# Optimization experiments

Measured on AMD Instinct MI355X. Metric: run time of the kernel, lower is better.

The kernel has to match this reference:

```python
import jax, jax.numpy as jnp
import numpy as np

B = 524288      # batch
CONT = 64       # continuous features
N_CATE = 16     # categorical fields
VOCAB = 1000    # vocab per field
EM = 8          # embedding dim
LOW = EM * N_CATE + CONT  # 192
R = 32          # representation dim
RH = 32         # rep hidden dim
PH = 16         # head hidden dim
N_HEAD = 8      # number of routing heads


def setup_inputs() -> dict:
    key = jax.random.key(0)
    ks = jax.random.split(key, 16)
    s = 0.05
    return {
        "x_cont": jax.random.normal(ks[0], (B, CONT), dtype=jnp.float32),
        "x_cate": jax.random.randint(ks[1], (B, N_CATE), 0, VOCAB, dtype=jnp.int64),
        "t": jax.random.randint(ks[2], (B, 1), 0, N_HEAD, dtype=jnp.int64),
        # embedding tables, one per categorical field
        "emb": jax.random.normal(ks[3], (N_CATE, VOCAB, EM), dtype=jnp.float32) * s,
        # representation DNN: LOW -> RH -> RH -> R (2 hidden layers + output)
        "W1": jax.random.normal(ks[4], (LOW, RH), dtype=jnp.float32) * s,
        "b1": jnp.zeros((RH,), dtype=jnp.float32),
        "W2": jax.random.normal(ks[5], (RH, RH), dtype=jnp.float32) * s,
        "b2": jnp.zeros((RH,), dtype=jnp.float32),
        "W3": jax.random.normal(ks[6], (RH, R), dtype=jnp.float32) * s,
        "b3": jnp.zeros((R,), dtype=jnp.float32),
        # stacked per-head DNNs: R -> PH -> 1 (1 hidden layer + output)
        "HW1": jax.random.normal(ks[7], (N_HEAD, R, PH), dtype=jnp.float32) * s,
        "Hb1": jnp.zeros((N_HEAD, PH), dtype=jnp.float32),
        "HW2": jax.random.normal(ks[8], (N_HEAD, PH, 1), dtype=jnp.float32) * s,
        "Hb2": jnp.zeros((N_HEAD, 1), dtype=jnp.float32),
    }


def reference(x_cont, x_cate, t, emb, W1, b1, W2, b2, W3, b3, HW1, Hb1, HW2, Hb2):
    # LowFeature: embed each categorical field and concat with continuous
    # emb[f, x_cate[:, f]] -> [B, N_CATE, EM]
    e = emb[jnp.arange(N_CATE)[None, :], x_cate]
    x = jnp.concatenate([x_cont, e.reshape(e.shape[0], -1)], axis=1)  # [B, LOW]
    # representation DNN (eval mode: dropout is identity)
    h = jax.nn.relu(x @ W1 + b1)
    h = jax.nn.relu(h @ W2 + b2)
    r = h @ W3 + b3  # [B, R]
    # evaluate all heads batched, then gather the routed head per sample
    hh = jax.nn.relu(jnp.einsum('br,nrh->bnh', r, HW1) + Hb1[None])  # [B, N_HEAD, PH]
    y_all = jnp.einsum('bnh,nho->bno', hh, HW2) + Hb2[None]          # [B, N_HEAD, 1]
    y = jnp.take_along_axis(y_all[..., 0], t, axis=1)[:, 0]          # [B]
    return y
```

## Files before the change

kernel.cpp:

```cpp
#include <hip/hip_runtime.h>

namespace {

typedef float  f32x4  __attribute__((ext_vector_type(4)));
typedef float  f32x16 __attribute__((ext_vector_type(16)));
typedef short  bf16x8 __attribute__((ext_vector_type(8)));
typedef int    i32x4  __attribute__((ext_vector_type(4)));
typedef unsigned int u32;

constexpr int kRows  = 524288;
constexpr int kCont  = 64;
constexpr int kNCate = 16;
constexpr int kVocab = 1000;
constexpr int kEm    = 8;
constexpr int kRH    = 32;
constexpr int kPH    = 16;

constexpr int    kNFrag = 48;
constexpr size_t kOffEH = (size_t)kNFrag * 1024;

__device__ inline u32 rne_hi(float x) {
    u32 u = __float_as_uint(x);
    return ((u + 0x7fffu + ((u >> 16) & 1u)) >> 16) & 0xffffu;
}
__device__ inline float hi_f32(u32 h) { return __uint_as_float(h << 16); }
__device__ inline u32 pack2(float a, float b) {
    return rne_hi(a) | (rne_hi(b) << 16);
}

union FragU { u32 w[4]; bf16x8 v; uint4 u4; };

__device__ inline f32x16 mfma16(bf16x8 a, bf16x8 b, f32x16 c) {
    return __builtin_amdgcn_mfma_f32_32x32x16_bf16(a, b, c, 0, 0, 0);
}
__device__ inline f32x16 zero16() {
    f32x16 z;
#pragma unroll
    for (int i = 0; i < 16; ++i) z[i] = 0.f;
    return z;
}
__device__ inline void gload_lds16(const void* g, void* l) {
    __builtin_amdgcn_global_load_lds(
        (const __attribute__((address_space(1))) void*)g,
        (__attribute__((address_space(3))) void*)l, 16, 0, 0);
}

__global__ __launch_bounds__(256) void build_wfrags(
    const float* __restrict__ W1, const float* __restrict__ W2,
    const float* __restrict__ W3, const float* __restrict__ HW1,
    ushort* __restrict__ WF)
{
    int gid = blockIdx.x * blockDim.x + threadIdx.x;
    if (gid >= kNFrag * 64) return;
    const int q = gid >> 6, l = gid & 63;
    const int lc = l & 31, g = l >> 5;

    const float* src; int k0, col, ldn, p;
    if (q < 12) {
        src = W1; col = lc; ldn = 32; p = 0;
        k0 = (q < 4) ? (16*q + 8*g) : (64 + 8*(q - 4) + 64*g);
    } else if (q < 24) {
        int f = q - 12;
        src = W1; col = lc; ldn = 32; p = 1;
        k0 = (f < 4) ? (16*f + 8*g) : (64 + 8*(f - 4) + 64*g);
    }
    else if (q < 28) { int u2 = q-24; src = W2; k0 = 16*(u2>>1) + 8*g; col = lc; ldn = 32; p = u2&1; }
    else if (q < 32) { int u2 = q-28; src = W3; k0 = 16*(u2>>1) + 8*g; col = lc; ldn = 32; p = u2&1; }
    else {
        int u2 = q-32; int n = u2>>2; int f = (u2>>1)&1; p = u2&1;
        int c128 = n*32 + lc; int head = c128 >> 4, ph = c128 & 15;
        src = HW1 + (size_t)head * kRH * kPH + ph;
        k0 = 16*f + 8*g; col = 0; ldn = kPH;
    }

    u32 hv[8];
#pragma unroll
    for (int j = 0; j < 8; ++j) {
        float w = src[(size_t)(k0 + j) * ldn + col];
        u32 h = rne_hi(w);
        hv[j] = (p == 0) ? h : rne_hi(w - hi_f32(h));
    }
    FragU fu;
#pragma unroll
    for (int w = 0; w < 4; ++w) fu.w[w] = hv[2*w] | (hv[2*w+1] << 16);
    ((uint4*)WF)[q * 64 + l] = fu.u4;
}

__global__ __launch_bounds__(256) void build_embhi(
    const float* __restrict__ emb, ushort* __restrict__ eh)
{
    int r = blockIdx.x * blockDim.x + threadIdx.x;
    if (r >= kNCate * kVocab) return;
    const float* e = emb + (size_t)r * kEm;
    FragU H;
#pragma unroll
    for (int w = 0; w < 4; ++w)
        H.w[w] = pack2(e[2*w], e[2*w+1]);
    ((uint4*)eh)[r] = H.u4;
}

__device__ inline void transition(const float* v, int g, FragU* H, FragU* L) {
    u32 hw[8], lw[8];
#pragma unroll
    for (int p = 0; p < 8; ++p) {
        float v0 = v[2*p], v1 = v[2*p+1];
        u32 h0 = rne_hi(v0), h1 = rne_hi(v1);
        hw[p] = h0 | (h1 << 16);
        lw[p] = pack2(v0 - hi_f32(h0), v1 - hi_f32(h1));
    }
#pragma unroll
    for (int f2 = 0; f2 < 2; ++f2) {
        u32 hp[4], lp[4];
#pragma unroll
        for (int p = 0; p < 4; ++p) {
            hp[p] = (u32)__shfl_xor((int)hw[4*f2 + p], 32);
            lp[p] = (u32)__shfl_xor((int)lw[4*f2 + p], 32);
        }
        H[f2].w[0] = g ? hp[2] : hw[4*f2+0];
        H[f2].w[1] = g ? hp[3] : hw[4*f2+1];
        H[f2].w[2] = g ? hw[4*f2+2] : hp[0];
        H[f2].w[3] = g ? hw[4*f2+3] : hp[1];
        L[f2].w[0] = g ? lp[2] : lw[4*f2+0];
        L[f2].w[1] = g ? lp[3] : lw[4*f2+1];
        L[f2].w[2] = g ? lw[4*f2+2] : lp[0];
        L[f2].w[3] = g ? lw[4*f2+3] : lp[1];
    }
}

__global__ __launch_bounds__(256, 2) void fused_main(
    const float* __restrict__ xc, const int* __restrict__ xcate,
    const int* __restrict__ tptr,
    const ushort* __restrict__ WF,
    const ushort* __restrict__ eh,
    const float* __restrict__ b1, const float* __restrict__ b2,
    const float* __restrict__ b3, const float* __restrict__ Hb1,
    const float* __restrict__ HW2, const float* __restrict__ Hb2,
    float* __restrict__ out)
{
    __shared__ __align__(16) uint4 sW4[16 * 64];
    __shared__ __align__(16) float sX[4][2048];
    __shared__ __align__(16) float sB[360];

    const int tid = threadIdx.x;
    const uint4* wf4 = (const uint4*)WF;

#pragma unroll
    for (int it = 0; it < 4; ++it) {
        const int i = tid + 256 * it;
        sW4[i] = wf4[i];
    }
    for (int i = tid; i < 360; i += 256) {
        float v;
        if      (i < 32)  v = b1[i];
        else if (i < 64)  v = b2[i - 32];
        else if (i < 96)  v = b3[i - 64];
        else if (i < 224) v = Hb1[i - 96];
        else if (i < 352) v = HW2[i - 224];
        else              v = Hb2[i - 352];
        sB[i] = v;
    }
    __syncthreads();

    const int wv = tid >> 6, l = tid & 63;
    const int lc = l & 31, g = l >> 5;
    const int tb = blockIdx.x * 128 + wv * 32;
    const int arow = tb + lc;

    char* xb = (char*)&sX[wv][0];
    {
        const float* xbase = xc + (size_t)tb * kCont;
#pragma unroll
        for (int i = 0; i < 8; ++i) {
            const int r   = 4*i + (l >> 4);
            const int c4s = (l & 15) ^ (r & 15);
            gload_lds16(xbase + r * kCont + c4s * 4, xb + i * 1024);
        }
    }

    i32x4 iq[2];
    {
        const i32x4* cr4 = (const i32x4*)(xcate + (size_t)arow * kNCate + 8*g);
        iq[0] = cr4[0];
        iq[1] = cr4[1];
    }
    const int t_lane = tptr[arow];

    uint4 ehv[8];
    {
        const uint4* eh4 = (const uint4*)eh;
#pragma unroll
        for (int i = 0; i < 8; ++i) {
            const int c   = i + 8*g;
            const int idx = (i < 4) ? iq[0][i] : iq[1][i - 4];
            ehv[i] = eh4[(size_t)(c * kVocab + idx)];
        }
    }

    asm volatile("s_waitcnt vmcnt(0)" ::: "memory");
    __builtin_amdgcn_sched_barrier(0);

    f32x16 acca = zero16(), accb = zero16();
#pragma unroll
    for (int f = 0; f < 4; ++f) {
        const int c0 = 4*f + 2*g;
        f32x4 va0 = *(const f32x4*)(xb + lc*256 + (((c0)     ^ (lc & 15)) * 16));
        f32x4 va1 = *(const f32x4*)(xb + lc*256 + (((c0 + 1) ^ (lc & 15)) * 16));
        FragU H, L;
#pragma unroll
        for (int w = 0; w < 4; ++w) {
            const f32x4& va = (w < 2) ? va0 : va1;
            const float v0 = va[2*(w & 1)], v1 = va[2*(w & 1) + 1];
            u32 h0 = rne_hi(v0), h1 = rne_hi(v1);
            H.w[w] = h0 | (h1 << 16);
            L.w[w] = pack2(v0 - hi_f32(h0), v1 - hi_f32(h1));
        }
        FragU WH, WL;
        WH.u4 = sW4[f * 64 + l];
        WL.u4 = sW4[(12 + f) * 64 + l];
        f32x16& acc = (f & 1) ? accb : acca;
        acc = mfma16(WH.v, H.v, acc);
        acc = mfma16(WL.v, H.v, acc);
        acc = mfma16(WH.v, L.v, acc);
    }
#pragma unroll
    for (int i = 0; i < 8; ++i) {
        const int f = 4 + i;
        FragU BH, WH;
        BH.u4 = ehv[i];
        WH.u4 = sW4[f * 64 + l];
        f32x16& acc = (f & 1) ? accb : acca;
        acc = mfma16(WH.v, BH.v, acc);
    }

    float v1v[16];
    {
#pragma unroll
        for (int p = 0; p < 4; ++p) {
            f32x4 bq = *(const f32x4*)&sB[0 + 8*p + 4*g];
#pragma unroll
            for (int m = 0; m < 4; ++m)
                v1v[4*p + m] = fmaxf(acca[4*p + m] + accb[4*p + m] + bq[m], 0.f);
        }
    }
    FragU a2h[2], a2l[2];
    transition(v1v, g, a2h, a2l);

    f32x16 acc2 = zero16();
#pragma unroll
    for (int f2 = 0; f2 < 2; ++f2) {
        FragU WH, WL;
        WH.u4 = wf4[(24 + 2*f2) * 64 + l];
        WL.u4 = wf4[(25 + 2*f2) * 64 + l];
        acc2 = mfma16(WH.v, a2h[f2].v, acc2);
        acc2 = mfma16(WL.v, a2h[f2].v, acc2);
        acc2 = mfma16(WH.v, a2l[f2].v, acc2);
    }
    float v2v[16];
    {
#pragma unroll
        for (int p = 0; p < 4; ++p) {
            f32x4 bq = *(const f32x4*)&sB[32 + 8*p + 4*g];
#pragma unroll
            for (int m = 0; m < 4; ++m)
                v2v[4*p + m] = fmaxf(acc2[4*p + m] + bq[m], 0.f);
        }
    }
    FragU a3h[2], a3l[2];
    transition(v2v, g, a3h, a3l);

    f32x16 acc3 = zero16();
#pragma unroll
    for (int f2 = 0; f2 < 2; ++f2) {
        FragU WH, WL;
        WH.u4 = wf4[(28 + 2*f2) * 64 + l];
        WL.u4 = wf4[(29 + 2*f2) * 64 + l];
        acc3 = mfma16(WH.v, a3h[f2].v, acc3);
        acc3 = mfma16(WL.v, a3h[f2].v, acc3);
        acc3 = mfma16(WH.v, a3l[f2].v, acc3);
    }
    float v3v[16];
    {
#pragma unroll
        for (int p = 0; p < 4; ++p) {
            f32x4 bq = *(const f32x4*)&sB[64 + 8*p + 4*g];
#pragma unroll
            for (int m = 0; m < 4; ++m)
                v3v[4*p + m] = acc3[4*p + m] + bq[m];
        }
    }
    FragU a4h[2], a4l[2];
    transition(v3v, g, a4h, a4l);

    const f32x4 hb1q0 = *(const f32x4*)&sB[96  + t_lane*16 + 4*g];
    const f32x4 hb1q1 = *(const f32x4*)&sB[96  + t_lane*16 + 8 + 4*g];
    const f32x4 hw2q0 = *(const f32x4*)&sB[224 + t_lane*16 + 4*g];
    const f32x4 hw2q1 = *(const f32x4*)&sB[224 + t_lane*16 + 8 + 4*g];

    float ys = 0.f;
#pragma unroll
    for (int n = 0; n < 4; ++n) {
        f32x16 hacc = zero16();
#pragma unroll
        for (int f2 = 0; f2 < 2; ++f2) {
            FragU WH, WL;
            WH.u4 = wf4[(32 + 4*n + 2*f2) * 64 + l];
            WL.u4 = wf4[(33 + 4*n + 2*f2) * 64 + l];
            hacc = mfma16(WH.v, a4h[f2].v, hacc);
            hacc = mfma16(WL.v, a4h[f2].v, hacc);
            hacc = mfma16(WH.v, a4l[f2].v, hacc);
        }
        const bool sel = ((t_lane >> 1) == n);
        const bool half = (t_lane & 1);
#pragma unroll
        for (int j = 0; j < 8; ++j) {
            const float bb = (j < 4) ? hb1q0[j] : hb1q1[j - 4];
            const float ww = (j < 4) ? hw2q0[j] : hw2q1[j - 4];
            const float c0 = fmaxf(hacc[j]     + bb, 0.f) * ww;
            const float c1 = fmaxf(hacc[8 + j] + bb, 0.f) * ww;
            const float pick = half ? c1 : c0;
            ys += sel ? pick : 0.f;
        }
    }

    const float ytot = ys + __shfl_xor(ys, 32);
    if (g == 0)
        out[arow] = ytot + sB[352 + t_lane];
}

}

extern "C" void kernel_launch(void* const* d_in, const int* in_sizes, int n_in,
                              void* d_out, int out_size, void* d_ws, size_t ws_size,
                              hipStream_t stream)
{
    const float* x_cont = (const float*)d_in[0];
    const int*   x_cate = (const int*)  d_in[1];
    const int*   t      = (const int*)  d_in[2];
    const float* emb    = (const float*)d_in[3];
    const float* W1     = (const float*)d_in[4];
    const float* b1     = (const float*)d_in[5];
    const float* W2     = (const float*)d_in[6];
    const float* b2     = (const float*)d_in[7];
    const float* W3     = (const float*)d_in[8];
    const float* b3     = (const float*)d_in[9];
    const float* HW1    = (const float*)d_in[10];
    const float* Hb1    = (const float*)d_in[11];
    const float* HW2    = (const float*)d_in[12];
    const float* Hb2    = (const float*)d_in[13];
    float* out = (float*)d_out;

    ushort* WF = (ushort*)d_ws;
    ushort* eh = (ushort*)((char*)d_ws + kOffEH);

    hipLaunchKernelGGL(build_wfrags, dim3(12), dim3(256), 0, stream, W1, W2, W3, HW1, WF);
    hipLaunchKernelGGL(build_embhi, dim3((kNCate*kVocab + 255)/256), dim3(256), 0, stream,
                       emb, eh);

    const int grid = kRows / 128;
    hipLaunchKernelGGL(fused_main, dim3(grid), dim3(256), 0, stream,
                       x_cont, x_cate, t, WF, eh,
                       b1, b2, b3, Hb1, HW2, Hb2, out);
}
```

Measured before the change: 77.38 us.

## Process two 32-row tiles per wave with software-pipelined prefetch

Each wave now handles two 32-row tiles. The x staging and index loads for the second tile are issued while the first tile is still computing, and the embedding gather for the second tile overlaps the first tile's later layers and head evaluation. The grid is halved, so the per-block weight and bias staging is amortized over twice as many rows, and the launch bound is raised to three blocks per CU. The extra in-flight registers for the second tile may raise register pressure or cause spills under the tighter occupancy bound.

```diff
diff --git a/kernel.cpp b/kernel.cpp
--- a/kernel.cpp
+++ b/kernel.cpp
@@ -43,6 +43,14 @@
     __builtin_amdgcn_global_load_lds(
         (const __attribute__((address_space(1))) void*)g,
         (__attribute__((address_space(3))) void*)l, 16, 0, 0);
+}
+__device__ inline void fence_vm0() {
+    asm volatile("s_waitcnt vmcnt(0)" ::: "memory");
+    __builtin_amdgcn_sched_barrier(0);
+}
+__device__ inline void fence_lgkm0() {
+    asm volatile("s_waitcnt lgkmcnt(0)" ::: "memory");
+    __builtin_amdgcn_sched_barrier(0);
 }
 
 __global__ __launch_bounds__(256) void build_wfrags(
@@ -127,7 +135,7 @@
     }
 }
 
-__global__ __launch_bounds__(256, 2) void fused_main(
+__global__ __launch_bounds__(256, 3) void fused_main(
     const float* __restrict__ xc, const int* __restrict__ xcate,
     const int* __restrict__ tptr,
     const ushort* __restrict__ WF,
@@ -163,77 +171,70 @@
 
     const int wv = tid >> 6, l = tid & 63;
     const int lc = l & 31, g = l >> 5;
-    const int tb = blockIdx.x * 128 + wv * 32;
-    const int arow = tb + lc;
-
+    const int rowbase = blockIdx.x * 256 + wv * 64;
     char* xb = (char*)&sX[wv][0];
-    {
-        const float* xbase = xc + (size_t)tb * kCont;
+    const uint4* eh4 = (const uint4*)eh;
+
+    auto stage_x = [&](int tbase) {
+        const float* xbase = xc + (size_t)tbase * kCont;
 #pragma unroll
         for (int i = 0; i < 8; ++i) {
             const int r   = 4*i + (l >> 4);
             const int c4s = (l & 15) ^ (r & 15);
             gload_lds16(xbase + r * kCont + c4s * 4, xb + i * 1024);
         }
-    }
-
-    i32x4 iq[2];
-    {
-        const i32x4* cr4 = (const i32x4*)(xcate + (size_t)arow * kNCate + 8*g);
+    };
+    auto load_idx = [&](int tbase, i32x4* iq, int& t_lane) {
+        const i32x4* cr4 = (const i32x4*)(xcate + (size_t)(tbase + lc) * kNCate + 8*g);
         iq[0] = cr4[0];
         iq[1] = cr4[1];
-    }
-    const int t_lane = tptr[arow];
-
-    uint4 ehv[8];
-    {
-        const uint4* eh4 = (const uint4*)eh;
+        t_lane = tptr[tbase + lc];
+    };
+    auto gather_emb = [&](const i32x4* iq, uint4* ehv) {
 #pragma unroll
         for (int i = 0; i < 8; ++i) {
             const int c   = i + 8*g;
             const int idx = (i < 4) ? iq[0][i] : iq[1][i - 4];
             ehv[i] = eh4[(size_t)(c * kVocab + idx)];
         }
-    }
-
-    asm volatile("s_waitcnt vmcnt(0)" ::: "memory");
-    __builtin_amdgcn_sched_barrier(0);
-
-    f32x16 acca = zero16(), accb = zero16();
-#pragma unroll
-    for (int f = 0; f < 4; ++f) {
-        const int c0 = 4*f + 2*g;
-        f32x4 va0 = *(const f32x4*)(xb + lc*256 + (((c0)     ^ (lc & 15)) * 16));
-        f32x4 va1 = *(const f32x4*)(xb + lc*256 + (((c0 + 1) ^ (lc & 15)) * 16));
-        FragU H, L;
-#pragma unroll
-        for (int w = 0; w < 4; ++w) {
-            const f32x4& va = (w < 2) ? va0 : va1;
-            const float v0 = va[2*(w & 1)], v1 = va[2*(w & 1) + 1];
-            u32 h0 = rne_hi(v0), h1 = rne_hi(v1);
-            H.w[w] = h0 | (h1 << 16);
-            L.w[w] = pack2(v0 - hi_f32(h0), v1 - hi_f32(h1));
-        }
-        FragU WH, WL;
-        WH.u4 = sW4[f * 64 + l];
-        WL.u4 = sW4[(12 + f) * 64 + l];
-        f32x16& acc = (f & 1) ? accb : acca;
-        acc = mfma16(WH.v, H.v, acc);
-        acc = mfma16(WL.v, H.v, acc);
-        acc = mfma16(WH.v, L.v, acc);
-    }
-#pragma unroll
-    for (int i = 0; i < 8; ++i) {
-        const int f = 4 + i;
-        FragU BH, WH;
-        BH.u4 = ehv[i];
-        WH.u4 = sW4[f * 64 + l];
-        f32x16& acc = (f & 1) ? accb : acca;
-        acc = mfma16(WH.v, BH.v, acc);
-    }
-
-    float v1v[16];
-    {
+    };
+    auto layer1_cont = [&](f32x16& acca, f32x16& accb) {
+#pragma unroll
+        for (int f = 0; f < 4; ++f) {
+            const int c0 = 4*f + 2*g;
+            f32x4 va0 = *(const f32x4*)(xb + lc*256 + (((c0)     ^ (lc & 15)) * 16));
+            f32x4 va1 = *(const f32x4*)(xb + lc*256 + (((c0 + 1) ^ (lc & 15)) * 16));
+            FragU H, L;
+#pragma unroll
+            for (int w = 0; w < 4; ++w) {
+                const f32x4& va = (w < 2) ? va0 : va1;
+                const float v0 = va[2*(w & 1)], v1 = va[2*(w & 1) + 1];
+                u32 h0 = rne_hi(v0), h1 = rne_hi(v1);
+                H.w[w] = h0 | (h1 << 16);
+                L.w[w] = pack2(v0 - hi_f32(h0), v1 - hi_f32(h1));
+            }
+            FragU WH, WL;
+            WH.u4 = sW4[f * 64 + l];
+            WL.u4 = sW4[(12 + f) * 64 + l];
+            f32x16& acc = (f & 1) ? accb : acca;
+            acc = mfma16(WH.v, H.v, acc);
+            acc = mfma16(WL.v, H.v, acc);
+            acc = mfma16(WH.v, L.v, acc);
+        }
+    };
+    auto layer1_emb = [&](const uint4* ehv, f32x16& acca, f32x16& accb) {
+#pragma unroll
+        for (int i = 0; i < 8; ++i) {
+            const int f = 4 + i;
+            FragU BH, WH;
+            BH.u4 = ehv[i];
+            WH.u4 = sW4[f * 64 + l];
+            f32x16& acc = (f & 1) ? accb : acca;
+            acc = mfma16(WH.v, BH.v, acc);
+        }
+    };
+    auto mid = [&](const f32x16& acca, const f32x16& accb, FragU* a4h, FragU* a4l) {
+        float v1v[16];
 #pragma unroll
         for (int p = 0; p < 4; ++p) {
             f32x4 bq = *(const f32x4*)&sB[0 + 8*p + 4*g];
@@ -241,22 +242,20 @@
             for (int m = 0; m < 4; ++m)
                 v1v[4*p + m] = fmaxf(acca[4*p + m] + accb[4*p + m] + bq[m], 0.f);
         }
-    }
-    FragU a2h[2], a2l[2];
-    transition(v1v, g, a2h, a2l);
-
-    f32x16 acc2 = zero16();
-#pragma unroll
-    for (int f2 = 0; f2 < 2; ++f2) {
-        FragU WH, WL;
-        WH.u4 = wf4[(24 + 2*f2) * 64 + l];
-        WL.u4 = wf4[(25 + 2*f2) * 64 + l];
-        acc2 = mfma16(WH.v, a2h[f2].v, acc2);
-        acc2 = mfma16(WL.v, a2h[f2].v, acc2);
-        acc2 = mfma16(WH.v, a2l[f2].v, acc2);
-    }
-    float v2v[16];
-    {
+        FragU a2h[2], a2l[2];
+        transition(v1v, g, a2h, a2l);
+
+        f32x16 acc2 = zero16();
+#pragma unroll
+        for (int f2 = 0; f2 < 2; ++f2) {
+            FragU WH, WL;
+            WH.u4 = wf4[(24 + 2*f2) * 64 + l];
+            WL.u4 = wf4[(25 + 2*f2) * 64 + l];
+            acc2 = mfma16(WH.v, a2h[f2].v, acc2);
+            acc2 = mfma16(WL.v, a2h[f2].v, acc2);
+            acc2 = mfma16(WH.v, a2l[f2].v, acc2);
+        }
+        float v2v[16];
 #pragma unroll
         for (int p = 0; p < 4; ++p) {
             f32x4 bq = *(const f32x4*)&sB[32 + 8*p + 4*g];
@@ -264,22 +263,20 @@
             for (int m = 0; m < 4; ++m)
                 v2v[4*p + m] = fmaxf(acc2[4*p + m] + bq[m], 0.f);
         }
-    }
-    FragU a3h[2], a3l[2];
-    transition(v2v, g, a3h, a3l);
-
-    f32x16 acc3 = zero16();
-#pragma unroll
-    for (int f2 = 0; f2 < 2; ++f2) {
-        FragU WH, WL;
-        WH.u4 = wf4[(28 + 2*f2) * 64 + l];
-        WL.u4 = wf4[(29 + 2*f2) * 64 + l];
-        acc3 = mfma16(WH.v, a3h[f2].v, acc3);
-        acc3 = mfma16(WL.v, a3h[f2].v, acc3);
-        acc3 = mfma16(WH.v, a3l[f2].v, acc3);
-    }
-    float v3v[16];
-    {
+        FragU a3h[2], a3l[2];
+        transition(v2v, g, a3h, a3l);
+
+        f32x16 acc3 = zero16();
+#pragma unroll
+        for (int f2 = 0; f2 < 2; ++f2) {
+            FragU WH, WL;
+            WH.u4 = wf4[(28 + 2*f2) * 64 + l];
+            WL.u4 = wf4[(29 + 2*f2) * 64 + l];
+            acc3 = mfma16(WH.v, a3h[f2].v, acc3);
+            acc3 = mfma16(WL.v, a3h[f2].v, acc3);
+            acc3 = mfma16(WH.v, a3l[f2].v, acc3);
+        }
+        float v3v[16];
 #pragma unroll
         for (int p = 0; p < 4; ++p) {
             f32x4 bq = *(const f32x4*)&sB[64 + 8*p + 4*g];
@@ -287,44 +284,79 @@
             for (int m = 0; m < 4; ++m)
                 v3v[4*p + m] = acc3[4*p + m] + bq[m];
         }
-    }
+        transition(v3v, g, a4h, a4l);
+    };
+    auto heads_store = [&](const FragU* a4h, const FragU* a4l, int t_lane, int arow) {
+        const f32x4 hb1q0 = *(const f32x4*)&sB[96  + t_lane*16 + 4*g];
+        const f32x4 hb1q1 = *(const f32x4*)&sB[96  + t_lane*16 + 8 + 4*g];
+        const f32x4 hw2q0 = *(const f32x4*)&sB[224 + t_lane*16 + 4*g];
+        const f32x4 hw2q1 = *(const f32x4*)&sB[224 + t_lane*16 + 8 + 4*g];
+
+        float ys = 0.f;
+#pragma unroll
+        for (int n = 0; n < 4; ++n) {
+            f32x16 hacc = zero16();
+#pragma unroll
+            for (int f2 = 0; f2 < 2; ++f2) {
+                FragU WH, WL;
+                WH.u4 = wf4[(32 + 4*n + 2*f2) * 64 + l];
+                WL.u4 = wf4[(33 + 4*n + 2*f2) * 64 + l];
+                hacc = mfma16(WH.v, a4h[f2].v, hacc);
+                hacc = mfma16(WL.v, a4h[f2].v, hacc);
+                hacc = mfma16(WH.v, a4l[f2].v, hacc);
+            }
+            const bool sel = ((t_lane >> 1) == n);
+            const bool half = (t_lane & 1);
+#pragma unroll
+            for (int j = 0; j < 8; ++j) {
+                const float bb = (j < 4) ? hb1q0[j] : hb1q1[j - 4];
+                const float ww = (j < 4) ? hw2q0[j] : hw2q1[j - 4];
+                const float c0 = fmaxf(hacc[j]     + bb, 0.f) * ww;
+                const float c1 = fmaxf(hacc[8 + j] + bb, 0.f) * ww;
+                const float pick = half ? c1 : c0;
+                ys += sel ? pick : 0.f;
+            }
+        }
+        const float ytot = ys + __shfl_xor(ys, 32);
+        if (g == 0)
+            out[arow] = ytot + sB[352 + t_lane];
+    };
+
+    const int tb1 = rowbase, tb2 = rowbase + 32;
+
+    stage_x(tb1);
+    i32x4 iq1[2]; int t1;
+    load_idx(tb1, iq1, t1);
+
+    fence_vm0();
+
+    uint4 ehv1[8];
+    gather_emb(iq1, ehv1);
+
+    f32x16 acca = zero16(), accb = zero16();
+    layer1_cont(acca, accb);
+
+    fence_lgkm0();
+    stage_x(tb2);
+    i32x4 iq2[2]; int t2;
+    load_idx(tb2, iq2, t2);
+
+    layer1_emb(ehv1, acca, accb);
     FragU a4h[2], a4l[2];
-    transition(v3v, g, a4h, a4l);
-
-    const f32x4 hb1q0 = *(const f32x4*)&sB[96  + t_lane*16 + 4*g];
-    const f32x4 hb1q1 = *(const f32x4*)&sB[96  + t_lane*16 + 8 + 4*g];
-    const f32x4 hw2q0 = *(const f32x4*)&sB[224 + t_lane*16 + 4*g];
-    const f32x4 hw2q1 = *(const f32x4*)&sB[224 + t_lane*16 + 8 + 4*g];
-
-    float ys = 0.f;
-#pragma unroll
-    for (int n = 0; n < 4; ++n) {
-        f32x16 hacc = zero16();
-#pragma unroll
-        for (int f2 = 0; f2 < 2; ++f2) {
-            FragU WH, WL;
-            WH.u4 = wf4[(32 + 4*n + 2*f2) * 64 + l];
-            WL.u4 = wf4[(33 + 4*n + 2*f2) * 64 + l];
-            hacc = mfma16(WH.v, a4h[f2].v, hacc);
-            hacc = mfma16(WL.v, a4h[f2].v, hacc);
-            hacc = mfma16(WH.v, a4l[f2].v, hacc);
-        }
-        const bool sel = ((t_lane >> 1) == n);
-        const bool half = (t_lane & 1);
-#pragma unroll
-        for (int j = 0; j < 8; ++j) {
-            const float bb = (j < 4) ? hb1q0[j] : hb1q1[j - 4];
-            const float ww = (j < 4) ? hw2q0[j] : hw2q1[j - 4];
-            const float c0 = fmaxf(hacc[j]     + bb, 0.f) * ww;
-            const float c1 = fmaxf(hacc[8 + j] + bb, 0.f) * ww;
-            const float pick = half ? c1 : c0;
-            ys += sel ? pick : 0.f;
-        }
-    }
-
-    const float ytot = ys + __shfl_xor(ys, 32);
-    if (g == 0)
-        out[arow] = ytot + sB[352 + t_lane];
+    mid(acca, accb, a4h, a4l);
+
+    uint4 ehv2[8];
+    gather_emb(iq2, ehv2);
+
+    heads_store(a4h, a4l, t1, tb1 + lc);
+
+    fence_vm0();
+
+    acca = zero16(); accb = zero16();
+    layer1_cont(acca, accb);
+    layer1_emb(ehv2, acca, accb);
+    mid(acca, accb, a4h, a4l);
+    heads_store(a4h, a4l, t2, tb2 + lc);
 }
 
 }
@@ -356,7 +388,7 @@
     hipLaunchKernelGGL(build_embhi, dim3((kNCate*kVocab + 255)/256), dim3(256), 0, stream,
                        emb, eh);
 
-    const int grid = kRows / 128;
+    const int grid = kRows / 256;
     hipLaunchKernelGGL(fused_main, dim3(grid), dim3(256), 0, stream,
                        x_cont, x_cate, t, WF, eh,
                        b1, b2, b3, Hb1, HW2, Hb2, out);
```

Result: faster. 74.98 us, median of 2 (-3.1%).
